# Kernel optimization log

Measured on AMD Instinct MI355X. Metric: run time of the kernel, lower is better.

The kernel has to match this reference:

```python
import jax, jax.numpy as jnp
import numpy as np

N_ATOMS = 100          # n_atoms from init_kwargs
BATCH = 1024           # dataset / batch size (single-batch usage per docstring)


def setup_inputs() -> dict:
    key = jax.random.key(0)
    k1, k2 = jax.random.split(key)
    # descriptors = pairwise distances between atoms -> 6 nonzero derivs per desc per frame
    ii, jj = np.triu_indices(N_ATOMS, 1)               # [D] each
    D = ii.shape[0]                                    # 4950 descriptors
    atoms = np.stack([ii, jj], axis=1)                 # [D, 2]
    atom_pd = np.repeat(atoms, 3, axis=1).reshape(-1)  # [D*6]: i,i,i,j,j,j per desc
    dim_pd = np.tile(np.array([0, 1, 2, 0, 1, 2]), D)  # [D*6]
    des_pd = np.repeat(np.arange(D), 6)                # [D*6]

    batch_ind = np.repeat(np.arange(BATCH), D * 6)     # [nnz]
    des_ind = np.tile(des_pd, BATCH)                   # [nnz]
    atom_ind = np.tile(atom_pd, BATCH)                 # [nnz]
    dim_ind = np.tile(dim_pd, BATCH)                   # [nnz]
    # faithful shifted index: per-frame offset + atom*3 + dim
    scatter_idx = batch_ind * (N_ATOMS * 3) + atom_ind * 3 + dim_ind

    nnz = batch_ind.shape[0]
    x = jax.random.normal(k1, (BATCH, D), dtype=jnp.float32)      # dq/d(descriptors)
    left = jax.random.normal(k2, (nnz,), dtype=jnp.float32)       # nonzero d(desc)/d(pos)
    return {
        "x": x,
        "left": left,
        "batch_ind": jnp.asarray(batch_ind, jnp.int32),
        "des_ind": jnp.asarray(des_ind, jnp.int32),
        "scatter_idx": jnp.asarray(scatter_idx, jnp.int32),
    }


def reference(x, left, batch_ind, des_ind, scatter_idx):
    # gather right operand: dq/d(desc) for each nonzero left entry
    right = x[batch_ind, des_ind]                      # [nnz]
    src = left * right                                 # chain rule terms
    # scatter-add into (frame, atom, dim) bins, then square (square modulus comps)
    acc = jax.ops.segment_sum(src, scatter_idx, num_segments=BATCH * N_ATOMS * 3)
    return (acc * acc).reshape(BATCH, N_ATOMS * 3)
```

## Files before the change

kernel.cpp:

```cpp
#include <hip/hip_runtime.h>


#define N_ATOMS 100
#define D_DESC  4950
#define BATCH   1024
#define NOUT    300
#define NWAVES  8

template<int CTRL, int RMASK>
__device__ __forceinline__ float dpp_step(float v) {
    int s = __builtin_amdgcn_update_dpp(0, __float_as_int(v), CTRL, RMASK, 0xf, true);
    return v + __int_as_float(s);
}
__device__ __forceinline__ float wave_sum(float v) {
    v = dpp_step<0x111, 0xf>(v);
    v = dpp_step<0x112, 0xf>(v);
    v = dpp_step<0x114, 0xf>(v);
    v = dpp_step<0x118, 0xf>(v);
    v = dpp_step<0x142, 0xa>(v);
    v = dpp_step<0x143, 0xc>(v);
    return v;
}

__global__ __launch_bounds__(512, 4)
void sd_kernel(const float* __restrict__ x,
               const float* __restrict__ left,
               float* __restrict__ out) {
    __shared__ float rowacc[NOUT];
    __shared__ float part[NWAVES][NOUT];
    const int b    = blockIdx.x;
    const int tid  = threadIdx.x;
    const int w    = tid >> 6;
    const int lane = tid & 63;

    for (int t = tid; t < NOUT; t += 512) rowacc[t] = 0.0f;
    __syncthreads();

    const float* __restrict__ xb = x    + (size_t)b * D_DESC;
    const float* __restrict__ lb = left + (size_t)b * D_DESC * 6;

    float a0 = 0.f, a1 = 0.f, a2 = 0.f;
    float b0 = 0.f, b1 = 0.f, b2 = 0.f;

    for (int i = w; i < N_ATOMS - 1; i += NWAVES) {
        const int base = (i * (2 * N_ATOMS - 1 - i)) >> 1;
        float s0 = 0.f, s1 = 0.f, s2 = 0.f;

        if (i < 63) {
            const int  j = lane;
            const bool v = j > i;
            const int  d = base + (v ? (j - i - 1) : 0);
            const float2* lp = (const float2*)(lb + (size_t)d * 6);
            const float2 c01 = lp[0];
            const float2 c23 = lp[1];
            const float2 c45 = lp[2];
            const float  xv  = xb[d];
            const float  m   = v ? xv : 0.f;
            s0 += c01.x * m;  s1 += c01.y * m;  s2 += c23.x * m;
            a0 += c23.y * m;  a1 += c45.x * m;  a2 += c45.y * m;
        }
        {
            const int  j = 64 + lane;
            const bool v = (j < N_ATOMS) && (j > i);
            const int  d = base + (v ? (j - i - 1) : 0);
            const float2* lp = (const float2*)(lb + (size_t)d * 6);
            const float2 c01 = lp[0];
            const float2 c23 = lp[1];
            const float2 c45 = lp[2];
            const float  xv  = xb[d];
            const float  m   = v ? xv : 0.f;
            s0 += c01.x * m;  s1 += c01.y * m;  s2 += c23.x * m;
            b0 += c23.y * m;  b1 += c45.x * m;  b2 += c45.y * m;
        }

        s0 = wave_sum(s0);
        s1 = wave_sum(s1);
        s2 = wave_sum(s2);
        if (lane == 63) {
            rowacc[i * 3 + 0] = s0;
            rowacc[i * 3 + 1] = s1;
            rowacc[i * 3 + 2] = s2;
        }
    }

    part[w][lane * 3 + 0] = a0;
    part[w][lane * 3 + 1] = a1;
    part[w][lane * 3 + 2] = a2;
    if (lane < N_ATOMS - 64) {
        part[w][(64 + lane) * 3 + 0] = b0;
        part[w][(64 + lane) * 3 + 1] = b1;
        part[w][(64 + lane) * 3 + 2] = b2;
    }
    __syncthreads();

    float* __restrict__ ob = out + (size_t)b * NOUT;
    for (int t = tid; t < NOUT; t += 512) {
        float v = rowacc[t];
        #pragma unroll
        for (int q = 0; q < NWAVES; ++q) v += part[q][t];
        ob[t] = v * v;
    }
}

extern "C" void kernel_launch(void* const* d_in, const int* in_sizes, int n_in,
                              void* d_out, int out_size, void* d_ws, size_t ws_size,
                              hipStream_t stream) {
    const float* x    = (const float*)d_in[0];
    const float* left = (const float*)d_in[1];
    float* out = (float*)d_out;
    sd_kernel<<<BATCH, 512, 0, stream>>>(x, left, out);
}
```

Before: 337.1 us.

## Stage left-operand rows into LDS with coalesced float4 loads per 8-row group

Each block now cooperatively copies the contiguous slice of `left` covering the next 8 atom rows into shared memory using float4 loads. Each wave then reads its row's derivative entries from LDS instead of issuing strided float2 global loads. Launch bounds are raised to target more blocks per CU. The cost is two block-wide barriers per group and about 18KB of extra LDS, which may limit occupancy and serialize the load and compute phases.

```diff
diff --git a/kernel.cpp b/kernel.cpp
--- a/kernel.cpp
+++ b/kernel.cpp
@@ -1,11 +1,17 @@
 #include <hip/hip_runtime.h>
 
 
-#define N_ATOMS 100
-#define D_DESC  4950
-#define BATCH   1024
-#define NOUT    300
-#define NWAVES  8
+#define N_ATOMS  100
+#define D_DESC   4950
+#define BATCH    1024
+#define NOUT     300
+#define NWAVES   8
+#define NGROUP   13
+#define STAGE_F4 1147
+
+__device__ __forceinline__ int rowstart(int i) {
+    return (i * (199 - i)) >> 1;
+}
 
 template<int CTRL, int RMASK>
 __device__ __forceinline__ float dpp_step(float v) {
@@ -22,65 +28,72 @@
     return v;
 }
 
-__global__ __launch_bounds__(512, 4)
+__global__ __launch_bounds__(512, 8)
 void sd_kernel(const float* __restrict__ x,
                const float* __restrict__ left,
                float* __restrict__ out) {
-    __shared__ float rowacc[NOUT];
-    __shared__ float part[NWAVES][NOUT];
+    __shared__ float4 stage[STAGE_F4];
+    __shared__ float  rowacc[NOUT];
+    __shared__ float  part[NWAVES][NOUT];
     const int b    = blockIdx.x;
     const int tid  = threadIdx.x;
     const int w    = tid >> 6;
     const int lane = tid & 63;
 
     for (int t = tid; t < NOUT; t += 512) rowacc[t] = 0.0f;
-    __syncthreads();
 
-    const float* __restrict__ xb = x    + (size_t)b * D_DESC;
-    const float* __restrict__ lb = left + (size_t)b * D_DESC * 6;
+    const float*  __restrict__ xb  = x + (size_t)b * D_DESC;
+    const float4* __restrict__ lb4 = (const float4*)(left + (size_t)b * D_DESC * 6);
 
     float a0 = 0.f, a1 = 0.f, a2 = 0.f;
     float b0 = 0.f, b1 = 0.f, b2 = 0.f;
 
-    for (int i = w; i < N_ATOMS - 1; i += NWAVES) {
-        const int base = (i * (2 * N_ATOMS - 1 - i)) >> 1;
-        float s0 = 0.f, s1 = 0.f, s2 = 0.f;
+    for (int g = 0; g < NGROUP; ++g) {
+        const int i0  = g * NWAVES;
+        const int rs0 = rowstart(i0);
+        const int rs8 = rowstart(min(i0 + NWAVES, N_ATOMS - 1));
+        const int f0 = (rs0 * 3) >> 1;
+        const int f1 = (rs8 * 3 + 1) >> 1;
+        for (int f = f0 + tid; f < f1; f += 512) stage[f - f0] = lb4[f];
+        __syncthreads();
 
-        if (i < 63) {
-            const int  j = lane;
-            const bool v = j > i;
-            const int  d = base + (v ? (j - i - 1) : 0);
-            const float2* lp = (const float2*)(lb + (size_t)d * 6);
-            const float2 c01 = lp[0];
-            const float2 c23 = lp[1];
-            const float2 c45 = lp[2];
-            const float  xv  = xb[d];
-            const float  m   = v ? xv : 0.f;
-            s0 += c01.x * m;  s1 += c01.y * m;  s2 += c23.x * m;
-            a0 += c23.y * m;  a1 += c45.x * m;  a2 += c45.y * m;
+        const int i = i0 + w;
+        if (i < N_ATOMS - 1) {
+            const int rs = rowstart(i);
+            const float* __restrict__ rowl = (const float*)stage + (rs * 6 - f0 * 4);
+            float s0 = 0.f, s1 = 0.f, s2 = 0.f;
+
+            if (i < 63) {
+                const int  j = lane;
+                const bool v = j > i;
+                const int  doff = v ? (j - i - 1) : 0;
+                const float2* lp = (const float2*)(rowl + doff * 6);
+                const float2 c01 = lp[0], c23 = lp[1], c45 = lp[2];
+                const float  m   = v ? xb[rs + doff] : 0.f;
+                s0 += c01.x * m;  s1 += c01.y * m;  s2 += c23.x * m;
+                a0 += c23.y * m;  a1 += c45.x * m;  a2 += c45.y * m;
+            }
+            {
+                const int  j = 64 + lane;
+                const bool v = (j < N_ATOMS) && (j > i);
+                const int  doff = v ? (j - i - 1) : 0;
+                const float2* lp = (const float2*)(rowl + doff * 6);
+                const float2 c01 = lp[0], c23 = lp[1], c45 = lp[2];
+                const float  m   = v ? xb[rs + doff] : 0.f;
+                s0 += c01.x * m;  s1 += c01.y * m;  s2 += c23.x * m;
+                b0 += c23.y * m;  b1 += c45.x * m;  b2 += c45.y * m;
+            }
+
+            s0 = wave_sum(s0);
+            s1 = wave_sum(s1);
+            s2 = wave_sum(s2);
+            if (lane == 63) {
+                rowacc[i * 3 + 0] = s0;
+                rowacc[i * 3 + 1] = s1;
+                rowacc[i * 3 + 2] = s2;
+            }
         }
-        {
-            const int  j = 64 + lane;
-            const bool v = (j < N_ATOMS) && (j > i);
-            const int  d = base + (v ? (j - i - 1) : 0);
-            const float2* lp = (const float2*)(lb + (size_t)d * 6);
-            const float2 c01 = lp[0];
-            const float2 c23 = lp[1];
-            const float2 c45 = lp[2];
-            const float  xv  = xb[d];
-            const float  m   = v ? xv : 0.f;
-            s0 += c01.x * m;  s1 += c01.y * m;  s2 += c23.x * m;
-            b0 += c23.y * m;  b1 += c45.x * m;  b2 += c45.y * m;
-        }
-
-        s0 = wave_sum(s0);
-        s1 = wave_sum(s1);
-        s2 = wave_sum(s2);
-        if (lane == 63) {
-            rowacc[i * 3 + 0] = s0;
-            rowacc[i * 3 + 1] = s1;
-            rowacc[i * 3 + 2] = s2;
-        }
+        __syncthreads();
     }
 
     part[w][lane * 3 + 0] = a0;
```

Result: no change. 339.7 us (+0.8%).
